# Optimization experiments

Hardware: AMD Instinct MI355X
Metric: run time of the kernel (lower is better)

The kernel has to match this reference:

```python
import jax, jax.numpy as jnp
import numpy as np

SIGMA = 1.0
KSIZE = 5
WEAK = 75.0
STRONG = 255.0
LOW_T = 0.00392
HIGH_T = 0.15

# scipy.signal.gaussian(M, std): unnormalized gaussian window
_n = np.arange(KSIZE, dtype=np.float32) - (KSIZE - 1) / 2.0
_g = np.exp(-0.5 * (_n / SIGMA) ** 2).astype(np.float32)
GAUSS_H = jnp.asarray(_g.reshape(1, 1, 1, KSIZE))  # horizontal 1xK
GAUSS_V = jnp.asarray(_g.reshape(1, 1, KSIZE, 1))  # vertical Kx1

_sobel = np.array([[1, 0, -1], [2, 0, -2], [1, 0, -1]], dtype=np.float32)
SOBEL_H = jnp.asarray(_sobel.reshape(1, 1, 3, 3))
SOBEL_V = jnp.asarray(_sobel.T.reshape(1, 1, 3, 3))

_f0 = np.array([[0, 0, 0], [0, 1, -1], [0, 0, 0]], np.float32)
_f45 = np.array([[0, 0, 0], [0, 1, 0], [0, 0, -1]], np.float32)
_f90 = np.array([[0, 0, 0], [0, 1, 0], [0, -1, 0]], np.float32)
_f135 = np.array([[0, 0, 0], [0, 1, 0], [-1, 0, 0]], np.float32)
_f180 = np.array([[0, 0, 0], [-1, 1, 0], [0, 0, 0]], np.float32)
_f225 = np.array([[-1, 0, 0], [0, 1, 0], [0, 0, 0]], np.float32)
_f270 = np.array([[0, -1, 0], [0, 1, 0], [0, 0, 0]], np.float32)
_f315 = np.array([[0, 0, -1], [0, 1, 0], [0, 0, 0]], np.float32)
DIR_FILT = jnp.asarray(np.stack([_f0, _f45, _f90, _f135, _f180, _f225, _f270, _f315]).reshape(8, 1, 3, 3))

NBR_FILT = jnp.asarray(np.array([[1, 1, 1], [1, 0, 1], [1, 1, 1]], np.float32).reshape(1, 1, 3, 3))


def _conv(x, w, pad):
    # cross-correlation, matching torch F.conv2d
    return jax.lax.conv_general_dilated(
        x, w, window_strides=(1, 1), padding=[(pad[0], pad[0]), (pad[1], pad[1])],
        dimension_numbers=('NCHW', 'OIHW', 'NCHW'))


def setup_inputs() -> dict:
    key = jax.random.key(0)
    img = jax.random.uniform(key, (16, 1, 1024, 1024), dtype=jnp.float32)
    return {"img": img}


def reference(img):
    B = img.shape[0]
    # --- gaussian noise removal (separable) ---
    sm = _conv(img, GAUSS_H, (0, KSIZE // 2))
    sm = _conv(sm, GAUSS_V, (KSIZE // 2, 0))
    # --- sobel gradients ---
    Ix = _conv(sm, SOBEL_H, (1, 1))
    Iy = _conv(sm, SOBEL_V, (1, 1))
    mag = jnp.sqrt(Ix ** 2 + Iy ** 2)
    mag = mag / mag.reshape(B, -1).max(axis=1).reshape(B, 1, 1, 1)
    direction = jnp.arctan2(Iy, Ix) * (180.0 / 3.1415926) + 180.0
    direction = jnp.round(direction / 45.0) * 45.0
    # --- non-max suppression via directional differences + gather ---
    all_filtered = _conv(mag, DIR_FILT, (1, 1))  # [B,8,H,W]
    idx_pos = (direction / 45.0).astype(jnp.int32) % 8  # [B,1,H,W]
    idx_neg = (idx_pos + 4) % 8
    cs_pos = jnp.take_along_axis(all_filtered, idx_pos, axis=1)
    cs_neg = jnp.take_along_axis(all_filtered, idx_neg, axis=1)
    is_max = jnp.minimum(cs_pos, cs_neg) > 0.0
    thin = jnp.where(is_max, mag, 0.0)
    # --- double threshold ---
    hi = thin.max() * HIGH_T  # global max, as in source
    strong = thin >= hi
    weak = (thin < hi) & (thin >= LOW_T)
    inter = jnp.where(strong, STRONG, jnp.where(weak, WEAK, 0.0))
    # --- hysteresis: iterate until no weak pixel gains a strong neighbor ---
    def cond(state):
        return state[1]

    def body(state):
        x, _ = state
        weak_m = x == WEAK
        sn = _conv((x == STRONG).astype(jnp.float32), NBR_FILT, (1, 1))
        new_strong = weak_m & (sn > 0.0)
        x = jnp.where(new_strong, STRONG, x)
        return x, new_strong.any()

    final, _ = jax.lax.while_loop(cond, body, (inter, jnp.asarray(True)))
    final = jnp.where(final == STRONG, final, 0.0)
    return final
```

## Files before the change

kernel.cpp:

```cpp
#include <hip/hip_runtime.h>
#include <math.h>

#define BB 16
#define H 1024
#define W 1024
#define HW (H*W)
#define NTOT (BB*HW)

typedef unsigned long long u64;

__device__ __constant__ float GW[5] = {
    0.13533528323661270f, 0.60653065971263342f, 1.0f,
    0.60653065971263342f, 0.13533528323661270f};

__device__ __constant__ int NBDY[8] = {0, 1, 1, 1, 0, -1, -1, -1};
__device__ __constant__ int NBDX[8] = {1, 1, 0, -1, -1, -1, 0, 1};

#define CSCALE ((float)(180.0 / 3.1415926))

#define TW 128
#define TH 8
__global__ __launch_bounds__(256, 8) void k_smooth_sobel(const float* __restrict__ img,
                                                         float* __restrict__ mag,
                                                         unsigned char* __restrict__ bucket,
                                                         float* __restrict__ partial) {
#pragma clang fp contract(off)
    __shared__ float sA[14 * 136 + 16];
    __shared__ float sB[14 * 132];
    __shared__ float red[256];

    const int tid = threadIdx.x;
    const int x0 = blockIdx.x * TW;
    const int y0 = blockIdx.y * TH;
    const int b = blockIdx.z;
    const size_t base = (size_t)b * HW;

    for (int idx = tid; idx < 14 * 34; idx += 256) {
        int r = idx / 34, v = idx - r * 34;
        int gy = y0 - 3 + r;
        int gxv = x0 - 4 + v * 4;
        float4 val = make_float4(0.f, 0.f, 0.f, 0.f);
        if (gy >= 0 && gy < H && gxv >= 0 && gxv <= W - 4)
            val = *(const float4*)&img[base + (size_t)gy * W + gxv];
        *(float4*)&sA[r * 136 + v * 4] = val;
    }
    __syncthreads();

    for (int idx = tid; idx < 14 * 33; idx += 256) {
        int r = idx / 33, g = idx - r * 33;
        const float* p = &sA[r * 136 + g * 4];
        float4 A0 = *(const float4*)p;
        float4 A1 = *(const float4*)(p + 4);
        float4 A2 = *(const float4*)(p + 8);
        float a_[12] = {A0.x, A0.y, A0.z, A0.w, A1.x, A1.y, A1.z, A1.w,
                        A2.x, A2.y, A2.z, A2.w};
        float o[4];
#pragma unroll
        for (int j = 0; j < 4; ++j) {
            float s = 0.0f;
#pragma unroll
            for (int k = 0; k < 5; ++k) s = s + GW[k] * a_[j + 1 + k];
            o[j] = s;
        }
        *(float4*)&sB[r * 132 + g * 4] = make_float4(o[0], o[1], o[2], o[3]);
    }
    __syncthreads();

    for (int idx = tid; idx < 10 * 33; idx += 256) {
        int rr = idx / 33, g = idx - rr * 33;
        float bb[20];
#pragma unroll
        for (int k = 0; k < 5; ++k) {
            float4 t = *(const float4*)&sB[(rr + k) * 132 + g * 4];
            bb[k * 4 + 0] = t.x; bb[k * 4 + 1] = t.y;
            bb[k * 4 + 2] = t.z; bb[k * 4 + 3] = t.w;
        }
        int gy = y0 - 1 + rr;
        bool rowok = (gy >= 0 && gy < H);
        float o[4];
#pragma unroll
        for (int j = 0; j < 4; ++j) {
            float s = 0.0f;
#pragma unroll
            for (int k = 0; k < 5; ++k) s = s + GW[k] * bb[k * 4 + j];
            int gx = x0 - 1 + g * 4 + j;
            o[j] = (rowok && gx >= 0 && gx < W) ? s : 0.0f;
        }
        *(float4*)&sA[rr * 136 + g * 4] = make_float4(o[0], o[1], o[2], o[3]);
    }
    __syncthreads();

    const int r = tid >> 5;
    const int cg = (tid & 31) * 4;
    const int y = y0 + r;
    const float* P0 = &sA[r * 136 + cg];
    const float* P1 = P0 + 136;
    const float* P2 = P1 + 136;
    float4 q0 = *(const float4*)P0; float2 e0 = *(const float2*)(P0 + 4);
    float4 q1 = *(const float4*)P1; float2 e1 = *(const float2*)(P1 + 4);
    float4 q2 = *(const float4*)P2; float2 e2 = *(const float2*)(P2 + 4);
    float r0[6] = {q0.x, q0.y, q0.z, q0.w, e0.x, e0.y};
    float r1[6] = {q1.x, q1.y, q1.z, q1.w, e1.x, e1.y};
    float r2[6] = {q2.x, q2.y, q2.z, q2.w, e2.x, e2.y};

    float tmax = 0.0f;
    float mg[4];
    unsigned int bk = 0;
#pragma unroll
    for (int j = 0; j < 4; ++j) {
        float a00 = r0[j], a01 = r0[j + 1], a02 = r0[j + 2];
        float a10 = r1[j],                  a12 = r1[j + 2];
        float a20 = r2[j], a21 = r2[j + 1], a22 = r2[j + 2];

        float Ix = a00;
        Ix = Ix - a02;
        Ix = Ix + 2.0f * a10;
        Ix = Ix - 2.0f * a12;
        Ix = Ix + a20;
        Ix = Ix - a22;

        float Iy = a00;
        Iy = Iy + 2.0f * a01;
        Iy = Iy + a02;
        Iy = Iy - a20;
        Iy = Iy - 2.0f * a21;
        Iy = Iy - a22;

        float t1 = Ix * Ix;
        float t2 = Iy * Iy;
        float m = sqrtf(t1 + t2);
        mg[j] = m;
        tmax = fmaxf(tmax, m);

        float ax = fabsf(Ix), ay = fabsf(Iy);
        float mn = fminf(ax, ay), mx = fmaxf(ax, ay);
        float cr = mn * 0.92387953f - mx * 0.38268343f;
        int bidx;
        if (fabsf(cr) < mx * 3e-5f) {
            float fa2 = (float)atan2((double)Iy, (double)Ix);
            float d2 = fa2 * CSCALE;
            d2 = d2 + 180.0f;
            float t2d = d2 / 45.0f;
            float rr2 = rintf(t2d);
            bidx = ((int)rr2) & 7;
        } else if (ay <= ax * 0.41421356f) {
            bidx = signbit(Ix) ? 0 : 4;
        } else if (ay >= ax * 2.41421356f) {
            bidx = (Iy >= 0.0f) ? 6 : 2;
        } else {
            bidx = (Iy >= 0.0f) ? ((Ix >= 0.0f) ? 5 : 7)
                                : ((Ix >= 0.0f) ? 3 : 1);
        }
        bk |= ((unsigned int)bidx) << (8 * j);
    }
    *(float4*)&mag[base + (size_t)y * W + x0 + cg] = make_float4(mg[0], mg[1], mg[2], mg[3]);
    *(unsigned int*)&bucket[base + (size_t)y * W + x0 + cg] = bk;

    red[tid] = tmax;
    __syncthreads();
    for (int s = 128; s > 0; s >>= 1) {
        if (tid < s) red[tid] = fmaxf(red[tid], red[tid + s]);
        __syncthreads();
    }
    if (tid == 0) {
        int pb = (blockIdx.z * 128 + blockIdx.y) * 8 + blockIdx.x;
        partial[pb] = red[0];
    }
}

__global__ __launch_bounds__(256) void k_redmax_img(const float* __restrict__ partial,
                                                    float* __restrict__ magmax) {
    __shared__ float red[256];
    const float* p = partial + blockIdx.x * 1024;
    float m = 0.0f;
    for (int k = threadIdx.x; k < 1024; k += 256) m = fmaxf(m, p[k]);
    red[threadIdx.x] = m;
    __syncthreads();
    for (int s = 128; s > 0; s >>= 1) {
        if (threadIdx.x < s) red[threadIdx.x] = fmaxf(red[threadIdx.x], red[threadIdx.x + s]);
        __syncthreads();
    }
    if (threadIdx.x == 0) magmax[blockIdx.x] = red[0];
}

__global__ __launch_bounds__(256, 6) void k_nms_b(const float* __restrict__ mag,
                                                  const unsigned char* __restrict__ bucket,
                                                  const float* __restrict__ magmax,
                                                  u64* __restrict__ Mb,
                                                  float* __restrict__ partial) {
#pragma clang fp contract(off)
    __shared__ float sN[34 * 136];
    __shared__ unsigned int nib32[256];
    __shared__ float red[256];

    const int tid = threadIdx.x;
    const int x0 = blockIdx.x * 128;
    const int y0 = blockIdx.y * 32;
    const int b = blockIdx.z;
    const size_t base = (size_t)b * HW;
    const float M = magmax[b];

    for (int idx = tid; idx < 34 * 34; idx += 256) {
        int r = idx / 34, v = idx - r * 34;
        int gy = y0 - 1 + r;
        int gxv = x0 - 4 + v * 4;
        float4 val = make_float4(0.f, 0.f, 0.f, 0.f);
        if (gy >= 0 && gy < H && gxv >= 0 && gxv <= W - 4)
            val = *(const float4*)&mag[base + (size_t)gy * W + gxv];
        *(float4*)&sN[r * 136 + v * 4] = val;
    }
    __syncthreads();

    const int r = tid >> 5;
    const int cg = (tid & 31) * 4;
    float amax = 0.0f;

    for (int k4 = 0; k4 < 4; ++k4) {
        const int rr = k4 * 8 + r;
        const int y = y0 + rr;
        unsigned int bk4 = *(const unsigned int*)&bucket[base + (size_t)y * W + x0 + cg];
        float4 a4 = *(const float4*)&sN[(rr + 1) * 136 + cg + 4];
        float av[4] = {a4.x, a4.y, a4.z, a4.w};
        bool im[4];
        bool bad = false;
        float bpv[4], bnv[4];
        bool g1v[4], g2v[4], f1v[4], f2v[4];
#pragma unroll
        for (int j = 0; j < 4; ++j) {
            int c = cg + j;
            int bkt = (bk4 >> (8 * j)) & 0xff;
            int dy = NBDY[bkt], dx = NBDX[bkt];
            float a = av[j];
            float bp = sN[(rr + 1 + dy) * 136 + c + 4 + dx];
            float bn = sN[(rr + 1 - dy) * 136 + c + 4 - dx];
            bpv[j] = bp; bnv[j] = bn;
            bool g1 = a > bp, g2 = a > bn;
            bool f1 = a >= bp * 1.0000005f;
            bool f2 = a >= bn * 1.0000005f;
            g1v[j] = g1; g2v[j] = g2; f1v[j] = f1; f2v[j] = f2;
            im[j] = g1 && g2;
            bad = bad || (g1 && !f1) || (g2 && !f2);
        }
        if (__any(bad)) {
#pragma unroll
            for (int j = 0; j < 4; ++j) {
                bool b1 = g1v[j] && !f1v[j];
                bool b2 = g2v[j] && !f2v[j];
                if (b1 || b2) {
                    float qa = av[j] / M;
                    bool r1 = g1v[j], r2 = g2v[j];
                    if (b1) r1 = qa > (bpv[j] / M);
                    if (b2) r2 = qa > (bnv[j] / M);
                    im[j] = r1 && r2;
                }
            }
        }
        unsigned int nib = 0;
#pragma unroll
        for (int j = 0; j < 4; ++j) {
            if (im[j]) { nib |= 1u << j; amax = fmaxf(amax, av[j]); }
        }
        nib32[tid] = nib;
        __syncthreads();
        if (tid < 16) {
            int rw = tid >> 1, h = tid & 1;
            u64 w = 0;
#pragma unroll
            for (int j = 0; j < 16; ++j)
                w |= (u64)nib32[rw * 32 + h * 16 + j] << (4 * j);
            int yy = y0 + k4 * 8 + rw;
            int widx = ((b << 8) | ((yy >> 6) << 4) | ((x0 >> 6) + h)) * 64 + (yy & 63);
            Mb[widx] = w;
        }
        __syncthreads();
    }

    red[tid] = amax;
    __syncthreads();
    for (int s = 128; s > 0; s >>= 1) {
        if (tid < s) red[tid] = fmaxf(red[tid], red[tid + s]);
        __syncthreads();
    }
    if (tid == 0)
        partial[(blockIdx.z * 32 + blockIdx.y) * 8 + blockIdx.x] = red[0] / M;
}

__global__ __launch_bounds__(1024) void k_finalize_thr(const float* __restrict__ partial,
                                                       float* __restrict__ hdr,
                                                       float* __restrict__ thr) {
    __shared__ float red[1024];
    float m = 0.0f;
    for (int k = threadIdx.x; k < 4096; k += 1024) m = fmaxf(m, partial[k]);
    red[threadIdx.x] = m;
    __syncthreads();
    for (int s = 512; s > 0; s >>= 1) {
        if (threadIdx.x < s) red[threadIdx.x] = fmaxf(red[threadIdx.x], red[threadIdx.x + s]);
        __syncthreads();
    }
    if (threadIdx.x == 0) hdr[16] = red[0];
    if (threadIdx.x < 32) {
        float tm = red[0];
        int t = threadIdx.x;
        float M = hdr[t >> 1];
        float T = (t & 1) ? (tm * 0.15f) : 0.00392f;
        if (0.0f / M >= T) { thr[t] = 0.0f; return; }
        unsigned int lo = 0u, hi = 0x7f800000u;
        while (hi - lo > 1u) {
            unsigned int mid = lo + ((hi - lo) >> 1);
            if (__uint_as_float(mid) / M >= T) hi = mid; else lo = mid;
        }
        thr[t] = __uint_as_float(hi);
    }
}

__global__ __launch_bounds__(256, 8) void k_thresh_b(const float* __restrict__ mag,
                                                     const u64* __restrict__ Mb,
                                                     const float* __restrict__ hdr,
                                                     const float* __restrict__ thr,
                                                     u64* __restrict__ Sb,
                                                     u64* __restrict__ Wb) {
    __shared__ unsigned int nibS[256], nibW[256];
    const int tid = threadIdx.x;
    const int x0 = blockIdx.x * 128;
    const int y0 = blockIdx.y * 32;
    const int b = blockIdx.z;
    const size_t base = (size_t)b * HW;
    const float Alo = thr[b * 2], Ahi = thr[b * 2 + 1];
    const bool snm = (hdr[16] * 0.15f <= 0.0f);
    const int r = tid >> 5;
    const int cg = (tid & 31) * 4;
    const int hl = cg >> 6;

    for (int k4 = 0; k4 < 4; ++k4) {
        const int rr = k4 * 8 + r;
        const int y = y0 + rr;
        float4 a4 = *(const float4*)&mag[base + (size_t)y * W + x0 + cg];
        float av[4] = {a4.x, a4.y, a4.z, a4.w};
        const int widx = ((b << 8) | ((y >> 6) << 4) | ((x0 >> 6) + hl)) * 64 + (y & 63);
        u64 mw = Mb[widx];
        unsigned int ns = 0, nw = 0;
#pragma unroll
        for (int j = 0; j < 4; ++j) {
            bool im = (mw >> ((cg & 63) + j)) & 1ull;
            bool strong = snm || (im && (av[j] >= Ahi));
            bool weak = (!strong) && im && (av[j] >= Alo);
            ns |= (strong ? 1u : 0u) << j;
            nw |= (weak ? 1u : 0u) << j;
        }
        nibS[tid] = ns;
        nibW[tid] = nw;
        __syncthreads();
        if (tid < 32) {
            bool isW = (tid >= 16);
            int t = tid & 15;
            int rw = t >> 1, h = t & 1;
            const unsigned int* nb = isW ? nibW : nibS;
            u64 w = 0;
#pragma unroll
            for (int j = 0; j < 16; ++j)
                w |= (u64)nb[rw * 32 + h * 16 + j] << (4 * j);
            int yy = y0 + k4 * 8 + rw;
            int widx2 = ((b << 8) | ((yy >> 6) << 4) | ((x0 >> 6) + h)) * 64 + (yy & 63);
            if (isW) Wb[widx2] = w; else Sb[widx2] = w;
        }
        __syncthreads();
    }
}

template <bool LAST>
__global__ __launch_bounds__(256) void k_hyster_bits(const u64* __restrict__ Wb,
                                                     u64* __restrict__ Sb,
                                                     float* __restrict__ out) {
    const int lane = threadIdx.x & 63;
    const int t = blockIdx.x * 4 + (threadIdx.x >> 6);
    const int ty = (t >> 4) & 15;
    const int tx = t & 15;
    const int idx = t * 64 + lane;

    u64 S = Sb[idx];
    const u64 Wk = Wb[idx];

    u64 hstat = 0;
    if (tx > 0)  hstat |= (Sb[(t - 1) * 64 + lane] >> 63) & 1ull;
    if (tx < 15) hstat |= (Sb[(t + 1) * 64 + lane] & 1ull) << 63;

    u64 halo = 0;
    if (lane == 0 && ty > 0) {
        const int ta = t - 16;
        u64 tc = Sb[ta * 64 + 63];
        u64 hh = (tc << 1) | tc | (tc >> 1);
        if (tx > 0)  hh |= (Sb[(ta - 1) * 64 + 63] >> 63) & 1ull;
        if (tx < 15) hh |= (Sb[(ta + 1) * 64 + 63] & 1ull) << 63;
        halo = hh;
    }
    if (lane == 63 && ty < 15) {
        const int tb = t + 16;
        u64 tc = Sb[tb * 64 + 0];
        u64 hh = (tc << 1) | tc | (tc >> 1);
        if (tx > 0)  hh |= (Sb[(tb - 1) * 64 + 0] >> 63) & 1ull;
        if (tx < 15) hh |= (Sb[(tb + 1) * 64 + 0] & 1ull) << 63;
        halo = hh;
    }

    for (int it = 0; it < 160; ++it) {
        u64 hh = (S << 1) | S | (S >> 1) | hstat;
        u64 up = __shfl_up(hh, 1, 64);
        if (lane == 0) up = halo;
        u64 dn = __shfl_down(hh, 1, 64);
        if (lane == 63) dn = halo;
        u64 dil = hh | up | dn;
        u64 nS = S | (Wk & dil);
        bool ch = (nS != S);
        S = nS;
        if (!__any(ch)) break;
    }

    if (!LAST) {
        Sb[idx] = S;
    } else {
        const int bimg = t >> 8;
        float* op = out + (size_t)bimg * HW + (size_t)(ty * 64) * W + tx * 64 + lane;
#pragma unroll 4
        for (int rr = 0; rr < 64; ++rr) {
            u64 wrow = __shfl(S, rr, 64);
            op[(size_t)rr * W] = ((wrow >> lane) & 1ull) ? 255.0f : 0.0f;
        }
    }
}

extern "C" void kernel_launch(void* const* d_in, const int* in_sizes, int n_in,
                              void* d_out, int out_size, void* d_ws, size_t ws_size,
                              hipStream_t stream) {
    (void)in_sizes; (void)n_in; (void)out_size; (void)ws_size;
    const float* img = (const float*)d_in[0];
    float* out = (float*)d_out;

    float* hdr = (float*)d_ws;
    float* thr = hdr + 64;
    float* partialA = hdr + 128;
    float* partialB = partialA + 16384;
    float* A = partialB + 4096;
    unsigned char* C = (unsigned char*)(A + (size_t)NTOT);
    u64* Sb = (u64*)(C + (size_t)NTOT);
    u64* Wb = Sb + NTOT / 64;
    u64* Mb = Wb + NTOT / 64;

    dim3 blk(256);
    k_smooth_sobel<<<dim3(8, 128, BB), blk, 0, stream>>>(img, A, C, partialA);
    k_redmax_img<<<dim3(BB), blk, 0, stream>>>(partialA, hdr);
    k_nms_b<<<dim3(8, 32, BB), blk, 0, stream>>>(A, C, hdr, Mb, partialB);
    k_finalize_thr<<<dim3(1), dim3(1024), 0, stream>>>(partialB, hdr, thr);
    k_thresh_b<<<dim3(8, 32, BB), blk, 0, stream>>>(A, Mb, hdr, thr, Sb, Wb);
    for (int p = 0; p < 5; ++p)
        k_hyster_bits<false><<<dim3(NTOT / (64 * 64) / 4), blk, 0, stream>>>(Wb, Sb, out);
    k_hyster_bits<true><<<dim3(NTOT / (64 * 64) / 4), blk, 0, stream>>>(Wb, Sb, out);
}
```

Measured before the change: 242.6 us.

## Rewrite NMS and threshold as wave-per-column streaming kernels with ballot bitpacking

The NMS and threshold kernels now assign one 64-wide wavefront to a 64x64 tile and stream down its rows. Each wave keeps a rolling three-row register window, gets horizontal neighbours through lane shuffles, and packs the result bits with __ballot. This removes the shared-memory tile staging, the nibble packing through shared memory and the block-wide syncs. The grid shrinks to 1024 blocks, each doing a 64-iteration serial loop. Loads are now scalar per lane instead of float4, and there is less parallelism to hide latency.

```diff
diff --git a/kernel.cpp b/kernel.cpp
--- a/kernel.cpp
+++ b/kernel.cpp
@@ -12,9 +12,6 @@
 __device__ __constant__ float GW[5] = {
     0.13533528323661270f, 0.60653065971263342f, 1.0f,
     0.60653065971263342f, 0.13533528323661270f};
-
-__device__ __constant__ int NBDY[8] = {0, 1, 1, 1, 0, -1, -1, -1};
-__device__ __constant__ int NBDX[8] = {1, 1, 0, -1, -1, -1, 0, 1};
 
 #define CSCALE ((float)(180.0 / 3.1415926))
 
@@ -183,96 +180,83 @@
     if (threadIdx.x == 0) magmax[blockIdx.x] = red[0];
 }
 
-__global__ __launch_bounds__(256, 6) void k_nms_b(const float* __restrict__ mag,
+__global__ __launch_bounds__(256, 8) void k_nms_s(const float* __restrict__ mag,
                                                   const unsigned char* __restrict__ bucket,
                                                   const float* __restrict__ magmax,
                                                   u64* __restrict__ Mb,
                                                   float* __restrict__ partial) {
 #pragma clang fp contract(off)
-    __shared__ float sN[34 * 136];
-    __shared__ unsigned int nib32[256];
     __shared__ float red[256];
-
     const int tid = threadIdx.x;
-    const int x0 = blockIdx.x * 128;
-    const int y0 = blockIdx.y * 32;
+    const int L = tid & 63, wv = tid >> 6;
+    const int sx = blockIdx.x * 4 + wv;
+    const int x0 = sx * 64;
+    const int y0 = blockIdx.y * 64;
     const int b = blockIdx.z;
     const size_t base = (size_t)b * HW;
     const float M = magmax[b];
-
-    for (int idx = tid; idx < 34 * 34; idx += 256) {
-        int r = idx / 34, v = idx - r * 34;
-        int gy = y0 - 1 + r;
-        int gxv = x0 - 4 + v * 4;
-        float4 val = make_float4(0.f, 0.f, 0.f, 0.f);
-        if (gy >= 0 && gy < H && gxv >= 0 && gxv <= W - 4)
-            val = *(const float4*)&mag[base + (size_t)gy * W + gxv];
-        *(float4*)&sN[r * 136 + v * 4] = val;
-    }
-    __syncthreads();
-
-    const int r = tid >> 5;
-    const int cg = (tid & 31) * 4;
+    const int x = x0 + L;
+    const int wbase = (((b << 8) | (blockIdx.y << 4) | sx)) * 64;
+
+    auto loadRow = [&](int y, float& Lv, float& Cv, float& Rv) {
+        float c = 0.0f, l = 0.0f, rr = 0.0f;
+        if (y >= 0 && y < H) {
+            c = mag[base + (size_t)y * W + x];
+            l = __shfl_up(c, 1);
+            rr = __shfl_down(c, 1);
+            if (L == 0)  l = (x0 > 0) ? mag[base + (size_t)y * W + (x0 - 1)] : 0.0f;
+            if (L == 63) rr = (x0 + 64 < W) ? mag[base + (size_t)y * W + (x0 + 64)] : 0.0f;
+        }
+        Lv = l; Cv = c; Rv = rr;
+    };
+
+    float pL, pC, pR, cL, cC, cR, nL, nC, nR, fL, fC, fR;
+    loadRow(y0 - 1, pL, pC, pR);
+    loadRow(y0, cL, cC, cR);
+    loadRow(y0 + 1, nL, nC, nR);
+
     float amax = 0.0f;
-
-    for (int k4 = 0; k4 < 4; ++k4) {
-        const int rr = k4 * 8 + r;
-        const int y = y0 + rr;
-        unsigned int bk4 = *(const unsigned int*)&bucket[base + (size_t)y * W + x0 + cg];
-        float4 a4 = *(const float4*)&sN[(rr + 1) * 136 + cg + 4];
-        float av[4] = {a4.x, a4.y, a4.z, a4.w};
-        bool im[4];
-        bool bad = false;
-        float bpv[4], bnv[4];
-        bool g1v[4], g2v[4], f1v[4], f2v[4];
-#pragma unroll
-        for (int j = 0; j < 4; ++j) {
-            int c = cg + j;
-            int bkt = (bk4 >> (8 * j)) & 0xff;
-            int dy = NBDY[bkt], dx = NBDX[bkt];
-            float a = av[j];
-            float bp = sN[(rr + 1 + dy) * 136 + c + 4 + dx];
-            float bn = sN[(rr + 1 - dy) * 136 + c + 4 - dx];
-            bpv[j] = bp; bnv[j] = bn;
-            bool g1 = a > bp, g2 = a > bn;
-            bool f1 = a >= bp * 1.0000005f;
-            bool f2 = a >= bn * 1.0000005f;
-            g1v[j] = g1; g2v[j] = g2; f1v[j] = f1; f2v[j] = f2;
-            im[j] = g1 && g2;
-            bad = bad || (g1 && !f1) || (g2 && !f2);
-        }
+    for (int i = 0; i < 64; ++i) {
+        int y = y0 + i;
+        loadRow(y + 2, fL, fC, fR);
+        int bkt = bucket[base + (size_t)y * W + x];
+        int t1 = (bkt + 1) & 7;
+        bool dyp = (bkt >= 1 && bkt <= 3);
+        bool dyn = (bkt >= 5);
+        bool dxp = (t1 <= 2);
+        bool dxn = (t1 >= 4 && t1 <= 6);
+
+        float rLv = dyn ? pL : (dyp ? nL : cL);
+        float rCv = dyn ? pC : (dyp ? nC : cC);
+        float rRv = dyn ? pR : (dyp ? nR : cR);
+        float bp = dxn ? rLv : (dxp ? rRv : rCv);
+        float sLv = dyn ? nL : (dyp ? pL : cL);
+        float sCv = dyn ? nC : (dyp ? pC : cC);
+        float sRv = dyn ? nR : (dyp ? pR : cR);
+        float bn = dxn ? sRv : (dxp ? sLv : sCv);
+
+        float a = cC;
+        bool g1 = a > bp, g2 = a > bn;
+        bool f1 = a >= bp * 1.0000005f;
+        bool f2 = a >= bn * 1.0000005f;
+        bool im = g1 && g2;
+        bool bad = (g1 && !f1) || (g2 && !f2);
         if (__any(bad)) {
-#pragma unroll
-            for (int j = 0; j < 4; ++j) {
-                bool b1 = g1v[j] && !f1v[j];
-                bool b2 = g2v[j] && !f2v[j];
-                if (b1 || b2) {
-                    float qa = av[j] / M;
-                    bool r1 = g1v[j], r2 = g2v[j];
-                    if (b1) r1 = qa > (bpv[j] / M);
-                    if (b2) r2 = qa > (bnv[j] / M);
-                    im[j] = r1 && r2;
-                }
+            if (bad) {
+                float qa = a / M;
+                bool r1 = g1, r2 = g2;
+                if (g1 && !f1) r1 = qa > (bp / M);
+                if (g2 && !f2) r2 = qa > (bn / M);
+                im = r1 && r2;
             }
         }
-        unsigned int nib = 0;
-#pragma unroll
-        for (int j = 0; j < 4; ++j) {
-            if (im[j]) { nib |= 1u << j; amax = fmaxf(amax, av[j]); }
-        }
-        nib32[tid] = nib;
-        __syncthreads();
-        if (tid < 16) {
-            int rw = tid >> 1, h = tid & 1;
-            u64 w = 0;
-#pragma unroll
-            for (int j = 0; j < 16; ++j)
-                w |= (u64)nib32[rw * 32 + h * 16 + j] << (4 * j);
-            int yy = y0 + k4 * 8 + rw;
-            int widx = ((b << 8) | ((yy >> 6) << 4) | ((x0 >> 6) + h)) * 64 + (yy & 63);
-            Mb[widx] = w;
-        }
-        __syncthreads();
+        if (im) amax = fmaxf(amax, a);
+        u64 word = __ballot(im);
+        if (L == 0) Mb[wbase + i] = word;
+
+        pL = cL; pC = cC; pR = cR;
+        cL = nL; cC = nC; cR = nR;
+        nL = fL; nC = fC; nR = fR;
     }
 
     red[tid] = amax;
@@ -282,15 +266,14 @@
         __syncthreads();
     }
     if (tid == 0)
-        partial[(blockIdx.z * 32 + blockIdx.y) * 8 + blockIdx.x] = red[0] / M;
+        partial[(blockIdx.z * 16 + blockIdx.y) * 4 + blockIdx.x] = red[0] / M;
 }
 
 __global__ __launch_bounds__(1024) void k_finalize_thr(const float* __restrict__ partial,
                                                        float* __restrict__ hdr,
                                                        float* __restrict__ thr) {
     __shared__ float red[1024];
-    float m = 0.0f;
-    for (int k = threadIdx.x; k < 4096; k += 1024) m = fmaxf(m, partial[k]);
+    float m = (threadIdx.x < 1024) ? partial[threadIdx.x] : 0.0f;
     red[threadIdx.x] = m;
     __syncthreads();
     for (int s = 512; s > 0; s >>= 1) {
@@ -313,57 +296,38 @@
     }
 }
 
-__global__ __launch_bounds__(256, 8) void k_thresh_b(const float* __restrict__ mag,
+__global__ __launch_bounds__(256, 8) void k_thresh_s(const float* __restrict__ mag,
                                                      const u64* __restrict__ Mb,
                                                      const float* __restrict__ hdr,
                                                      const float* __restrict__ thr,
                                                      u64* __restrict__ Sb,
                                                      u64* __restrict__ Wb) {
-    __shared__ unsigned int nibS[256], nibW[256];
     const int tid = threadIdx.x;
-    const int x0 = blockIdx.x * 128;
-    const int y0 = blockIdx.y * 32;
+    const int L = tid & 63, wv = tid >> 6;
+    const int sx = blockIdx.x * 4 + wv;
+    const int x0 = sx * 64;
+    const int y0 = blockIdx.y * 64;
     const int b = blockIdx.z;
     const size_t base = (size_t)b * HW;
     const float Alo = thr[b * 2], Ahi = thr[b * 2 + 1];
     const bool snm = (hdr[16] * 0.15f <= 0.0f);
-    const int r = tid >> 5;
-    const int cg = (tid & 31) * 4;
-    const int hl = cg >> 6;
-
-    for (int k4 = 0; k4 < 4; ++k4) {
-        const int rr = k4 * 8 + r;
-        const int y = y0 + rr;
-        float4 a4 = *(const float4*)&mag[base + (size_t)y * W + x0 + cg];
-        float av[4] = {a4.x, a4.y, a4.z, a4.w};
-        const int widx = ((b << 8) | ((y >> 6) << 4) | ((x0 >> 6) + hl)) * 64 + (y & 63);
-        u64 mw = Mb[widx];
-        unsigned int ns = 0, nw = 0;
-#pragma unroll
-        for (int j = 0; j < 4; ++j) {
-            bool im = (mw >> ((cg & 63) + j)) & 1ull;
-            bool strong = snm || (im && (av[j] >= Ahi));
-            bool weak = (!strong) && im && (av[j] >= Alo);
-            ns |= (strong ? 1u : 0u) << j;
-            nw |= (weak ? 1u : 0u) << j;
-        }
-        nibS[tid] = ns;
-        nibW[tid] = nw;
-        __syncthreads();
-        if (tid < 32) {
-            bool isW = (tid >= 16);
-            int t = tid & 15;
-            int rw = t >> 1, h = t & 1;
-            const unsigned int* nb = isW ? nibW : nibS;
-            u64 w = 0;
-#pragma unroll
-            for (int j = 0; j < 16; ++j)
-                w |= (u64)nb[rw * 32 + h * 16 + j] << (4 * j);
-            int yy = y0 + k4 * 8 + rw;
-            int widx2 = ((b << 8) | ((yy >> 6) << 4) | ((x0 >> 6) + h)) * 64 + (yy & 63);
-            if (isW) Wb[widx2] = w; else Sb[widx2] = w;
-        }
-        __syncthreads();
+    const int wbase = (((b << 8) | (blockIdx.y << 4) | sx)) * 64;
+
+    float a_nxt = mag[base + (size_t)y0 * W + x0 + L];
+    u64 mw_nxt = Mb[wbase];
+    for (int i = 0; i < 64; ++i) {
+        float a = a_nxt;
+        u64 mw = mw_nxt;
+        if (i < 63) {
+            a_nxt = mag[base + (size_t)(y0 + i + 1) * W + x0 + L];
+            mw_nxt = Mb[wbase + i + 1];
+        }
+        bool im = (mw >> L) & 1ull;
+        bool strong = snm || (im && (a >= Ahi));
+        bool weak = (!strong) && im && (a >= Alo);
+        u64 sw = __ballot(strong);
+        u64 ww = __ballot(weak);
+        if (L == 0) { Sb[wbase + i] = sw; Wb[wbase + i] = ww; }
     }
 }
 
@@ -448,9 +412,9 @@
     dim3 blk(256);
     k_smooth_sobel<<<dim3(8, 128, BB), blk, 0, stream>>>(img, A, C, partialA);
     k_redmax_img<<<dim3(BB), blk, 0, stream>>>(partialA, hdr);
-    k_nms_b<<<dim3(8, 32, BB), blk, 0, stream>>>(A, C, hdr, Mb, partialB);
+    k_nms_s<<<dim3(4, 16, BB), blk, 0, stream>>>(A, C, hdr, Mb, partialB);
     k_finalize_thr<<<dim3(1), dim3(1024), 0, stream>>>(partialB, hdr, thr);
-    k_thresh_b<<<dim3(8, 32, BB), blk, 0, stream>>>(A, Mb, hdr, thr, Sb, Wb);
+    k_thresh_s<<<dim3(4, 16, BB), blk, 0, stream>>>(A, Mb, hdr, thr, Sb, Wb);
     for (int p = 0; p < 5; ++p)
         k_hyster_bits<false><<<dim3(NTOT / (64 * 64) / 4), blk, 0, stream>>>(Wb, Sb, out);
     k_hyster_bits<true><<<dim3(NTOT / (64 * 64) / 4), blk, 0, stream>>>(Wb, Sb, out);
```

Result: slower. 293.3 us (+20.9%).
